# Optimization experiments

Measured on AMD Instinct MI355X. Metric: run time of the kernel, lower is better.

## Reference

```python
import jax, jax.numpy as jnp
import numpy as np

B, CIN, COUT, K, L = 32, 128, 128, 7, 4096
STRIDE, PAD = 1, 3
TEMP = 1.0


def setup_inputs() -> dict:
    key = jax.random.key(0)
    k1, k2 = jax.random.split(key)
    x = jax.random.normal(k1, (B, CIN, L), dtype=jnp.float32)
    weight = jax.random.normal(k2, (COUT, CIN, K), dtype=jnp.float32) * 0.1  # init: normal(0, 0.1)
    bias = jnp.zeros((COUT,), dtype=jnp.float32)
    return {"x": x, "weight": weight, "bias": bias}


def reference(x, weight, bias):
    # Soft tropical conv (intended math of the module):
    #   y[b,o,w] = T * logsumexp_{c,k}( (x[b,c,w*stride+k] + W[o,c,k]) / T ) + bias[o]
    # with -inf padding (exp(-inf)=0 => plain zero padding in exp space).
    # Computed as a numerically-stabilized standard conv in exp space, which is
    # mathematically identical and avoids materializing the (B,O,C,K,L) tensor.
    xm = jnp.max(x)
    wm = jnp.max(weight)
    ex = jnp.exp((x - xm) / TEMP)          # (B, CIN, L)
    ew = jnp.exp((weight - wm) / TEMP)     # (COUT, CIN, K)
    s = jax.lax.conv_general_dilated(
        ex, ew,
        window_strides=(STRIDE,),
        padding=[(PAD, PAD)],
        dimension_numbers=("NCH", "OIH", "NCH"),
    )  # (B, COUT, L_out); cross-correlation, matching torch unfold indexing x[i+k]
    y = TEMP * jnp.log(s) + (xm + wm)
    return y + bias[None, :, None]
```

## Files before the change

kernel.cpp:

```cpp
#include <hip/hip_runtime.h>
#include <hip/hip_bf16.h>
#include <cstdint>
#include <cstddef>

#define B_N   32
#define CIN_  128
#define COUT_ 128
#define KW_   7
#define L_    4096
#define PAD_  3
#define NW_   256
#define RPB   4104
#define NWELEM (KW_ * COUT_ * CIN_)
#define NGUARD (B_N * 8 * CIN_)

#define SX_ROWS  264
#define SX_ELEMS (SX_ROWS * CIN_)

typedef __attribute__((ext_vector_type(8))) short  bf16x8;
typedef __attribute__((ext_vector_type(4))) float  f32x4;

__device__ __forceinline__ void gl2lds16(const void* g, void* l) {
    __builtin_amdgcn_global_load_lds(
        (const __attribute__((address_space(1))) unsigned int*)g,
        (__attribute__((address_space(3))) unsigned int*)l, 16, 0, 0);
}

__global__ __launch_bounds__(256) void exp_x_kernel(
        const float* __restrict__ x, __hip_bfloat16* __restrict__ exT,
        const float* __restrict__ w, __hip_bfloat16* __restrict__ ewb) {
    if (blockIdx.x >= 64) {
        if (blockIdx.y != 0) return;
        int base = (blockIdx.x - 64) * 256 + threadIdx.x;
        #pragma unroll
        for (int i = 0; i < 32; ++i) {
            int idx = base + 4608 * i;
            if (idx < NWELEM) {
                int e  = idx & 7;
                int li = (idx >> 3) & 63;
                int cc = (idx >> 9) & 3;
                int blk = idx >> 11;
                int og = blk & 7, t = blk >> 3;
                int o  = og * 16 + (li & 15);
                int ch = cc * 32 + ((li >> 4) << 3) + e;
                ewb[idx] = __float2bfloat16(__expf(w[(o * CIN_ + ch) * KW_ + t]));
            } else {
                int j  = idx - NWELEM;
                int b  = j >> 10, rr = (j >> 7) & 7, c = j & 127;
                int r  = (rr < 3) ? rr : (4096 + rr);
                exT[((size_t)b * RPB + r) * CIN_ + c] = __float2bfloat16(0.0f);
            }
        }
        return;
    }

    __shared__ __align__(16) __hip_bfloat16 tileT[64 * 136];
    const int b  = blockIdx.y;
    const int l0 = blockIdx.x * 64;
    const int tid = threadIdx.x;
    const float* xb = x + (size_t)b * CIN_ * L_ + l0;

    #pragma unroll
    for (int i = 0; i < 8; ++i) {
        int idx = tid + 256 * i;
        int c   = idx >> 4;
        int lv4 = (idx & 15) * 4;
        f32x4 v = *(const f32x4*)(xb + (size_t)c * L_ + lv4);
        #pragma unroll
        for (int k2 = 0; k2 < 4; ++k2) {
            int l  = lv4 + k2;
            int sw = (l >> 2) & 15;
            tileT[l * 136 + (c ^ (sw << 3))] = __float2bfloat16(__expf(v[k2]));
        }
    }
    __syncthreads();

    __hip_bfloat16* dst = exT + ((size_t)b * RPB + l0 + PAD_) * CIN_;
    #pragma unroll
    for (int i = 0; i < 4; ++i) {
        int idx = tid + 256 * i;
        int l  = idx >> 4;
        int gc = idx & 15;
        int sw = (l >> 2) & 15;
        bf16x8 vv = *(const bf16x8*)&tileT[l * 136 + ((gc ^ sw) << 3)];
        *(bf16x8*)(dst + (size_t)l * CIN_ + gc * 8) = vv;
    }
}

__global__ __launch_bounds__(256, 2) void tropconv_kernel(
        const __hip_bfloat16* __restrict__ exT,
        const __hip_bfloat16* __restrict__ ewb,
        const float* __restrict__ bias,
        float* __restrict__ out) {
    __shared__ __align__(16) __hip_bfloat16 sX[SX_ELEMS];

    const int tid  = threadIdx.x;
    const int lane = tid & 63;
    const int wave = tid >> 6;
    const int wm   = wave >> 1;
    const int wn   = wave & 1;
    const int l15  = lane & 15;
    const int q    = lane >> 4;

    const int b  = blockIdx.y;
    const int w0 = blockIdx.x * NW_;
    const __hip_bfloat16* exb = exT + ((size_t)b * RPB + w0) * CIN_;

    #pragma unroll
    for (int s = 0; s < 16; ++s) {
        int gx = tid + 256 * s;
        int p = gx >> 4, j = gx & 15;
        gl2lds16(exb + (p << 7) + ((j ^ (p & 7)) << 3), &sX[gx * 8]);
    }
    if (tid < 128) {
        int gx = tid + 4096;
        int p = gx >> 4, j = gx & 15;
        gl2lds16(exb + (p << 7) + ((j ^ (p & 7)) << 3), &sX[gx * 8]);
    }

    f32x4 acc[4][8];
    #pragma unroll
    for (int i = 0; i < 4; ++i)
        #pragma unroll
        for (int j = 0; j < 8; ++j)
            acc[i][j] = (f32x4){0.f, 0.f, 0.f, 0.f};

    __syncthreads();

#define ALOAD(AF, T, CC)                                                     \
    do {                                                                     \
        _Pragma("unroll")                                                    \
        for (int mi = 0; mi < 4; ++mi)                                       \
            AF[mi] = *(const bf16x8*)&ewb[(((((T) * 8 + wm * 4 + mi) * 4     \
                                             + (CC)) << 6) + lane) * 8];     \
    } while (0)

#define BDOT(AF, T, CC)                                                      \
    do {                                                                     \
        bf16x8 bx[8];                                                        \
        _Pragma("unroll")                                                    \
        for (int ni = 0; ni < 8; ++ni) {                                     \
            int p = wn * 128 + ni * 16 + l15 + (T);                          \
            int g = ((CC) * 4 + q) ^ (p & 7);                                \
            bx[ni] = *(const bf16x8*)&sX[(p << 7) + (g << 3)];               \
        }                                                                    \
        __builtin_amdgcn_s_setprio(1);                                       \
        _Pragma("unroll")                                                    \
        for (int mi = 0; mi < 4; ++mi)                                       \
            _Pragma("unroll")                                                \
            for (int ni = 0; ni < 8; ++ni)                                   \
                acc[mi][ni] = __builtin_amdgcn_mfma_f32_16x16x32_bf16(       \
                    AF[mi], bx[ni], acc[mi][ni], 0, 0, 0);                   \
        __builtin_amdgcn_s_setprio(0);                                       \
    } while (0)

    {
        bf16x8 afA[4], afB[4];
        ALOAD(afA, 0, 0);
        ALOAD(afB, 1, 0);  BDOT(afA, 0, 0);
        ALOAD(afA, 2, 0);  BDOT(afB, 1, 0);
        ALOAD(afB, 3, 0);  BDOT(afA, 2, 0);
        ALOAD(afA, 4, 0);  BDOT(afB, 3, 0);
        ALOAD(afB, 5, 0);  BDOT(afA, 4, 0);
        ALOAD(afA, 6, 0);  BDOT(afB, 5, 0);
        ALOAD(afB, 0, 1);  BDOT(afA, 6, 0);
        ALOAD(afA, 1, 1);  BDOT(afB, 0, 1);
        ALOAD(afB, 2, 1);  BDOT(afA, 1, 1);
        ALOAD(afA, 3, 1);  BDOT(afB, 2, 1);
        ALOAD(afB, 4, 1);  BDOT(afA, 3, 1);
        ALOAD(afA, 5, 1);  BDOT(afB, 4, 1);
        ALOAD(afB, 6, 1);  BDOT(afA, 5, 1);
        ALOAD(afA, 0, 2);  BDOT(afB, 6, 1);
        ALOAD(afB, 1, 2);  BDOT(afA, 0, 2);
        ALOAD(afA, 2, 2);  BDOT(afB, 1, 2);
        ALOAD(afB, 3, 2);  BDOT(afA, 2, 2);
        ALOAD(afA, 4, 2);  BDOT(afB, 3, 2);
        ALOAD(afB, 5, 2);  BDOT(afA, 4, 2);
        ALOAD(afA, 6, 2);  BDOT(afB, 5, 2);
        ALOAD(afB, 0, 3);  BDOT(afA, 6, 2);
        ALOAD(afA, 1, 3);  BDOT(afB, 0, 3);
        ALOAD(afB, 2, 3);  BDOT(afA, 1, 3);
        ALOAD(afA, 3, 3);  BDOT(afB, 2, 3);
        ALOAD(afB, 4, 3);  BDOT(afA, 3, 3);
        ALOAD(afA, 5, 3);  BDOT(afB, 4, 3);
        ALOAD(afB, 6, 3);  BDOT(afA, 5, 3);
                           BDOT(afB, 6, 3);
    }
#undef ALOAD
#undef BDOT

    float* outb = out + (size_t)b * COUT_ * L_;
    #pragma unroll
    for (int mi = 0; mi < 4; ++mi) {
        #pragma unroll
        for (int r = 0; r < 4; ++r) {
            int o = wm * 64 + mi * 16 + q * 4 + r;
            float bv = bias[o];
            #pragma unroll
            for (int ni = 0; ni < 8; ++ni) {
                int w = w0 + wn * 128 + ni * 16 + l15;
                outb[(size_t)o * L_ + w] = __logf(acc[mi][ni][r]) + bv;
            }
        }
    }
}

extern "C" void kernel_launch(void* const* d_in, const int* in_sizes, int n_in,
                              void* d_out, int out_size, void* d_ws, size_t ws_size,
                              hipStream_t stream) {
    const float* x    = (const float*)d_in[0];
    const float* wgt  = (const float*)d_in[1];
    const float* bias = (const float*)d_in[2];
    float* out = (float*)d_out;

    __hip_bfloat16* exT = (__hip_bfloat16*)d_ws;
    __hip_bfloat16* ewb = (__hip_bfloat16*)((char*)d_ws + (size_t)B_N * RPB * CIN_ * 2);

    exp_x_kernel<<<dim3(64 + 18, B_N), 256, 0, stream>>>(x, exT, wgt, ewb);
    tropconv_kernel<<<dim3(L_ / NW_, B_N), 256, 0, stream>>>(exT, ewb, bias, out);
}
```

Measured before the change: 143.9 us.

## Fuse exp and transpose of x into conv kernel, drop intermediate buffer

The separate pass that exponentiated x, transposed it to channel-last bf16 and wrote it to workspace is removed. The conv kernel now reads fp32 x directly, applies exp, handles padding with zeros, and scatters bf16 values into a swizzled LDS tile. A new swizzle pattern is used for both the writes and the MFMA operand reads. This saves a full global round trip of the exp'd activations and one kernel's worth of work, but adds per-block exp compute, scalar 2-byte LDS stores, and some halo recomputation.

```diff
diff --git a/kernel.cpp b/kernel.cpp
--- a/kernel.cpp
+++ b/kernel.cpp
@@ -8,11 +8,8 @@
 #define COUT_ 128
 #define KW_   7
 #define L_    4096
-#define PAD_  3
 #define NW_   256
-#define RPB   4104
 #define NWELEM (KW_ * COUT_ * CIN_)
-#define NGUARD (B_N * 8 * CIN_)
 
 #define SX_ROWS  264
 #define SX_ELEMS (SX_ROWS * CIN_)
@@ -20,75 +17,25 @@
 typedef __attribute__((ext_vector_type(8))) short  bf16x8;
 typedef __attribute__((ext_vector_type(4))) float  f32x4;
 
-__device__ __forceinline__ void gl2lds16(const void* g, void* l) {
-    __builtin_amdgcn_global_load_lds(
-        (const __attribute__((address_space(1))) unsigned int*)g,
-        (__attribute__((address_space(3))) unsigned int*)l, 16, 0, 0);
-}
-
-__global__ __launch_bounds__(256) void exp_x_kernel(
-        const float* __restrict__ x, __hip_bfloat16* __restrict__ exT,
+__global__ __launch_bounds__(256) void prep_w_kernel(
         const float* __restrict__ w, __hip_bfloat16* __restrict__ ewb) {
-    if (blockIdx.x >= 64) {
-        if (blockIdx.y != 0) return;
-        int base = (blockIdx.x - 64) * 256 + threadIdx.x;
-        #pragma unroll
-        for (int i = 0; i < 32; ++i) {
-            int idx = base + 4608 * i;
-            if (idx < NWELEM) {
-                int e  = idx & 7;
-                int li = (idx >> 3) & 63;
-                int cc = (idx >> 9) & 3;
-                int blk = idx >> 11;
-                int og = blk & 7, t = blk >> 3;
-                int o  = og * 16 + (li & 15);
-                int ch = cc * 32 + ((li >> 4) << 3) + e;
-                ewb[idx] = __float2bfloat16(__expf(w[(o * CIN_ + ch) * KW_ + t]));
-            } else {
-                int j  = idx - NWELEM;
-                int b  = j >> 10, rr = (j >> 7) & 7, c = j & 127;
-                int r  = (rr < 3) ? rr : (4096 + rr);
-                exT[((size_t)b * RPB + r) * CIN_ + c] = __float2bfloat16(0.0f);
-            }
-        }
-        return;
-    }
-
-    __shared__ __align__(16) __hip_bfloat16 tileT[64 * 136];
-    const int b  = blockIdx.y;
-    const int l0 = blockIdx.x * 64;
-    const int tid = threadIdx.x;
-    const float* xb = x + (size_t)b * CIN_ * L_ + l0;
-
-    #pragma unroll
-    for (int i = 0; i < 8; ++i) {
-        int idx = tid + 256 * i;
-        int c   = idx >> 4;
-        int lv4 = (idx & 15) * 4;
-        f32x4 v = *(const f32x4*)(xb + (size_t)c * L_ + lv4);
-        #pragma unroll
-        for (int k2 = 0; k2 < 4; ++k2) {
-            int l  = lv4 + k2;
-            int sw = (l >> 2) & 15;
-            tileT[l * 136 + (c ^ (sw << 3))] = __float2bfloat16(__expf(v[k2]));
-        }
-    }
-    __syncthreads();
-
-    __hip_bfloat16* dst = exT + ((size_t)b * RPB + l0 + PAD_) * CIN_;
+    int base = blockIdx.x * 1024 + threadIdx.x;
     #pragma unroll
     for (int i = 0; i < 4; ++i) {
-        int idx = tid + 256 * i;
-        int l  = idx >> 4;
-        int gc = idx & 15;
-        int sw = (l >> 2) & 15;
-        bf16x8 vv = *(const bf16x8*)&tileT[l * 136 + ((gc ^ sw) << 3)];
-        *(bf16x8*)(dst + (size_t)l * CIN_ + gc * 8) = vv;
+        int idx = base + 256 * i;
+        int e  = idx & 7;
+        int li = (idx >> 3) & 63;
+        int cc = (idx >> 9) & 3;
+        int blk = idx >> 11;
+        int og = blk & 7, t = blk >> 3;
+        int o  = og * 16 + (li & 15);
+        int ch = cc * 32 + ((li >> 4) << 3) + e;
+        ewb[idx] = __float2bfloat16(__expf(w[(o * CIN_ + ch) * KW_ + t]));
     }
 }
 
 __global__ __launch_bounds__(256, 2) void tropconv_kernel(
-        const __hip_bfloat16* __restrict__ exT,
+        const float* __restrict__ x,
         const __hip_bfloat16* __restrict__ ewb,
         const float* __restrict__ bias,
         float* __restrict__ out) {
@@ -104,18 +51,32 @@
 
     const int b  = blockIdx.y;
     const int w0 = blockIdx.x * NW_;
-    const __hip_bfloat16* exb = exT + ((size_t)b * RPB + w0) * CIN_;
+    const float* xb = x + (size_t)b * CIN_ * L_;
 
     #pragma unroll
-    for (int s = 0; s < 16; ++s) {
-        int gx = tid + 256 * s;
-        int p = gx >> 4, j = gx & 15;
-        gl2lds16(exb + (p << 7) + ((j ^ (p & 7)) << 3), &sX[gx * 8]);
-    }
-    if (tid < 128) {
-        int gx = tid + 4096;
-        int p = gx >> 4, j = gx & 15;
-        gl2lds16(exb + (p << 7) + ((j ^ (p & 7)) << 3), &sX[gx * 8]);
+    for (int i = 0; i < 8; ++i) {
+        int idx = tid + 256 * i;
+        int c   = idx >> 4;
+        int gb  = idx & 15;
+        int cHi = c >> 3, cLo = c & 7;
+        #pragma unroll
+        for (int j = 0; j < 5; ++j) {
+            int g = gb + 16 * j;
+            if (g >= 66) continue;
+            int l0  = w0 - 4 + 4 * g;
+            int l0c = min(max(l0, 0), L_ - 4);
+            f32x4 v = *(const f32x4*)(xb + (size_t)c * L_ + l0c);
+            #pragma unroll
+            for (int e = 0; e < 4; ++e) {
+                int l = l0 + e;
+                int p = 4 * g + e - 1;
+                if ((unsigned)p < 262u) {
+                    float val = ((unsigned)l < (unsigned)L_) ? __expf(v[e]) : 0.0f;
+                    int slot = cHi ^ ((p ^ (p >> 2)) & 7);
+                    sX[(p << 7) + (slot << 3) + cLo] = __float2bfloat16(val);
+                }
+            }
+        }
     }
 
     f32x4 acc[4][8];
@@ -141,7 +102,7 @@
         _Pragma("unroll")                                                    \
         for (int ni = 0; ni < 8; ++ni) {                                     \
             int p = wn * 128 + ni * 16 + l15 + (T);                          \
-            int g = ((CC) * 4 + q) ^ (p & 7);                                \
+            int g = ((CC) * 4 + q) ^ ((p ^ (p >> 2)) & 7);                   \
             bx[ni] = *(const bf16x8*)&sX[(p << 7) + (g << 3)];               \
         }                                                                    \
         __builtin_amdgcn_s_setprio(1);                                       \
@@ -213,9 +174,8 @@
     const float* bias = (const float*)d_in[2];
     float* out = (float*)d_out;
 
-    __hip_bfloat16* exT = (__hip_bfloat16*)d_ws;
-    __hip_bfloat16* ewb = (__hip_bfloat16*)((char*)d_ws + (size_t)B_N * RPB * CIN_ * 2);
+    __hip_bfloat16* ewb = (__hip_bfloat16*)d_ws;
 
-    exp_x_kernel<<<dim3(64 + 18, B_N), 256, 0, stream>>>(x, exT, wgt, ewb);
-    tropconv_kernel<<<dim3(L_ / NW_, B_N), 256, 0, stream>>>(exT, ewb, bias, out);
+    prep_w_kernel<<<NWELEM / 1024, 256, 0, stream>>>(wgt, ewb);
+    tropconv_kernel<<<dim3(L_ / NW_, B_N), 256, 0, stream>>>(x, ewb, bias, out);
 }
```

Result: slower. 176.0 us (+22.3%).
